# Kernel tuning notes

Hardware: AMD Instinct MI355X
Metric: run time of the kernel (lower is better)

## Reference

```python
import jax, jax.numpy as jnp
import numpy as np

B, S, D, H, HID = 2, 2048, 256, 8, 1024
EPS = 1e-9


def gelu_fast(x):
    return 0.5 * x * (1.0 + jnp.tanh(x * 0.7978845608 * (1.0 + 0.044715 * x * x)))


def layer_norm(x, g, b):
    m = jnp.mean(x, axis=-1, keepdims=True)
    v = jnp.mean(jnp.square(x - m), axis=-1, keepdims=True)
    return (x - m) * jax.lax.rsqrt(v + EPS) * g + b


def setup_inputs() -> dict:
    key = jax.random.key(0)
    ks = jax.random.split(key, 16)
    x = jax.random.normal(ks[0], (B, S, D), dtype=jnp.float32)
    # causal look-ahead mask: additive, 0 on/below diagonal, -1e9 above
    causal = jnp.triu(jnp.ones((S, S), dtype=jnp.float32), k=1) * (-1e9)
    look_ahead_mask = causal[None, None, :, :]  # (1,1,S,S)
    sd = 0.02
    return {
        "x": x,
        "look_ahead_mask": look_ahead_mask,
        "ln1_g": jnp.ones((D,), jnp.float32),
        "ln1_b": jnp.zeros((D,), jnp.float32),
        "wq_w": jax.random.normal(ks[1], (D * H, D), jnp.float32) * sd,
        "wq_b": jnp.zeros((D * H,), jnp.float32),
        "wk_w": jax.random.normal(ks[2], (D * H, D), jnp.float32) * sd,
        "wk_b": jnp.zeros((D * H,), jnp.float32),
        "wv_w": jax.random.normal(ks[3], (D * H, D), jnp.float32) * sd,
        "wv_b": jnp.zeros((D * H,), jnp.float32),
        "dense_w": jax.random.normal(ks[4], (D, D * H), jnp.float32) * sd,
        "dense_b": jnp.zeros((D,), jnp.float32),
        "ln2_g": jnp.ones((D,), jnp.float32),
        "ln2_b": jnp.zeros((D,), jnp.float32),
        "fc1_w": jax.random.normal(ks[5], (HID, D), jnp.float32) * sd,
        "fc1_b": jnp.zeros((HID,), jnp.float32),
        "fc2_w": jax.random.normal(ks[6], (D, HID), jnp.float32) * sd,
        "fc2_b": jnp.zeros((D,), jnp.float32),
    }


def reference(x, look_ahead_mask, ln1_g, ln1_b, wq_w, wq_b, wk_w, wk_b,
              wv_w, wv_b, dense_w, dense_b, ln2_g, ln2_b,
              fc1_w, fc1_b, fc2_w, fc2_b):
    xn = layer_norm(x, ln1_g, ln1_b)
    # QKV: D -> D*H, each head has full head-dim D (module quirk)
    q = (jnp.einsum('bsd,ed->bse', xn, wq_w) + wq_b).reshape(B, S, H, D).transpose(0, 2, 1, 3)
    k = (jnp.einsum('bsd,ed->bse', xn, wk_w) + wk_b).reshape(B, S, H, D).transpose(0, 2, 1, 3)
    v = (jnp.einsum('bsd,ed->bse', xn, wv_w) + wv_b).reshape(B, S, H, D).transpose(0, 2, 1, 3)
    scores = jnp.einsum('bhqd,bhkd->bhqk', q, k) / jnp.sqrt(jnp.float32(D))
    scores = scores + look_ahead_mask
    attn_weights = jax.nn.softmax(scores, axis=-1)
    ctx = jnp.einsum('bhqk,bhkd->bhqd', attn_weights, v)  # (B,H,S,D)
    ctx = ctx.transpose(0, 2, 1, 3).reshape(B, S, H * D)
    attn = jnp.einsum('bse,de->bsd', ctx, dense_w) + dense_b
    x1 = xn + attn  # residual uses post-LN x (module quirk)
    m = layer_norm(x1, ln2_g, ln2_b)
    m = gelu_fast(jnp.einsum('bsd,hd->bsh', m, fc1_w) + fc1_b)
    m = jnp.einsum('bsh,dh->bsd', m, fc2_w) + fc2_b
    out = x1 + m
    return out, attn_weights
```

## Files before the change

### kernel.cpp

```cpp
#include <hip/hip_runtime.h>
#include <hip/hip_bf16.h>


typedef __bf16 bf16_t;
typedef __bf16 bf16x8 __attribute__((ext_vector_type(8)));
typedef __bf16 bf16x4 __attribute__((ext_vector_type(4)));
typedef float  f32x4  __attribute__((ext_vector_type(4)));

#define DEV __device__ __forceinline__

DEV f32x4 mfma16(bf16x8 a, bf16x8 b, f32x4 c) {
  return __builtin_amdgcn_mfma_f32_16x16x32_bf16(a, b, c, 0, 0, 0);
}

DEV void gload16(const void* g, void* l) {
  __builtin_amdgcn_global_load_lds(
      (const __attribute__((address_space(1))) unsigned int*)g,
      (__attribute__((address_space(3))) unsigned int*)l, 16, 0, 0);
}

__global__ __launch_bounds__(256) void k1_lncvt(
    const float* __restrict__ x, const float* __restrict__ g, const float* __restrict__ bta,
    float* __restrict__ of, bf16_t* __restrict__ ob,
    const float* __restrict__ s0, const float* __restrict__ s1,
// ... 88 lines not shown
__global__ __launch_bounds__(256, 4) void gemm_qkv(
    const bf16_t* __restrict__ A,
    const bf16_t* __restrict__ W0, const bf16_t* __restrict__ W1, const bf16_t* __restrict__ W2,
    const float* __restrict__ b0, const float* __restrict__ b1, const float* __restrict__ b2,
    bf16_t* __restrict__ qo, bf16_t* __restrict__ ko, bf16_t* __restrict__ vto) {
  __shared__ char smem[34816];
  char* Asb = smem;
  char* Bsb = smem + 16384;
  int bx = blockIdx.x;
  int wsel = bx >> 4, cb = bx & 15;
  const bf16_t* W    = wsel == 0 ? W0 : (wsel == 1 ? W1 : W2);
  const float*  bias = wsel == 0 ? b0 : (wsel == 1 ? b1 : b2);
  int row0 = blockIdx.y * 128, col0 = cb * 128;
  f32x4 acc[4][4] = {};
  gemm_core(A, W, 256, row0, col0, 0, 8, Asb, Bsb, acc);

  int tid = threadIdx.x, w = tid >> 6, l = tid & 63, l15 = l & 15, lhi = l >> 4;
  int wr = (w >> 1) * 64, wc = (w & 1) * 64;

  if (wsel < 2) {
    bf16_t* out = wsel == 0 ? qo : ko;
#pragma unroll
    for (int m = 0; m < 4; ++m)
#pragma unroll
      for (int n = 0; n < 4; ++n)
#pragma unroll
        for (int j = 0; j < 4; ++j) {
          int row = row0 + wr + 16 * m + lhi * 4 + j;
          int col = col0 + wc + 16 * n + l15;
          float v = acc[m][n][j] + bias[col];
          out[((size_t)((row >> 11) * 8 + (col >> 8)) * 2048 + (row & 2047)) * 256 + (col & 255)] = (bf16_t)v;
        }
  } else {
    __syncthreads();
    bf16_t* T = (bf16_t*)smem;
#pragma unroll
    for (int m = 0; m < 4; ++m)
#pragma unroll
      for (int n = 0; n < 4; ++n) {
        int d = wc + 16 * n + l15;
        int s = wr + 16 * m + lhi * 4;
        bf16x4 v4;
#pragma unroll
        for (int j = 0; j < 4; ++j) v4[j] = (bf16_t)(acc[m][n][j] + bias[col0 + d]);
        *(bf16x4*)(T + d * 136 + s) = v4;
      }
    __syncthreads();
    int bh = ((row0 >> 11) << 3) + (col0 >> 8);
    int d0 = col0 & 255, s0g = row0 & 2047;
#pragma unroll
    for (int p = 0; p < 8; ++p) {
      int idx = p * 256 + tid;
      int d = idx >> 4, c = (idx & 15) * 8;
      bf16x8 v8 = *(const bf16x8*)(T + d * 136 + c);
      *(bf16x8*)(vto + ((size_t)bh * 256 + d0 + d) * 2048 + s0g + c) = v8;
    }
  }
}

__global__ __launch_bounds__(256, 4) void gemm_part(
    const bf16_t* __restrict__ A, const bf16_t* __restrict__ W,
    int lda, int ksub, float* __restrict__ parts) {
  __shared__ char Asb[2 * 8192];
  __shared__ char Bsb[2 * 8192];
  int z = blockIdx.z;
  int row0 = blockIdx.y * 128, col0 = blockIdx.x * 128;
  f32x4 acc[4][4] = {};
  gemm_core(A, W, lda, row0, col0, z * ksub, ksub >> 5, Asb, Bsb, acc);

  int tid = threadIdx.x, w = tid >> 6, l = tid & 63, l15 = l & 15, lhi = l >> 4;
  int wr = (w >> 1) * 64, wc = (w & 1) * 64;
  float* p = parts + (size_t)z * 1048576;
#pragma unroll
  for (int m = 0; m < 4; ++m)
#pragma unroll
    for (int n = 0; n < 4; ++n)
#pragma unroll
      for (int j = 0; j < 4; ++j) {
        int row = row0 + wr + 16 * m + lhi * 4 + j;
        int col = col0 + wc + 16 * n + l15;
        p[(size_t)row * 256 + col] = acc[m][n][j];
      }
}

__global__ __launch_bounds__(256) void reduce4(
    const float* __restrict__ parts, const float* __restrict__ bias,
    const float* __restrict__ res, float* __restrict__ out) {
  int i = blockIdx.x * 256 + threadIdx.x;
  f32x4 s = *(const f32x4*)(parts + (size_t)i * 4);
  s += *(const f32x4*)(parts + 1048576 + (size_t)i * 4);
  s += *(const f32x4*)(parts + 2097152 + (size_t)i * 4);
  s += *(const f32x4*)(parts + 3145728 + (size_t)i * 4);
  s += *(const f32x4*)(res + (size_t)i * 4);
  s += *(const f32x4*)(bias + (i & 63) * 4);
  *(f32x4*)(out + (size_t)i * 4) = s;
}

__global__ __launch_bounds__(256) void reduce_ln(
    const float* __restrict__ parts, const float* __restrict__ bias,
    const float* __restrict__ res, const float* __restrict__ g,
    const float* __restrict__ bta, float* __restrict__ x1o, bf16_t* __restrict__ mo) {
  int row = blockIdx.x * 4 + (threadIdx.x >> 6);
  int l = threadIdx.x & 63;
  size_t base = (size_t)row * 256 + l * 4;
  f32x4 s = *(const f32x4*)(parts + base);
  s += *(const f32x4*)(parts + 1048576 + base);
  s += *(const f32x4*)(parts + 2097152 + base);
  s += *(const f32x4*)(parts + 3145728 + base);
  s += *(const f32x4*)(res + base);
  s += *(const f32x4*)(bias + l * 4);
  *(f32x4*)(x1o + base) = s;
  float sm = s[0] + s[1] + s[2] + s[3];
  float s2 = s[0]*s[0] + s[1]*s[1] + s[2]*s[2] + s[3]*s[3];
#pragma unroll
  for (int o = 1; o < 64; o <<= 1) { sm += __shfl_xor(sm, o, 64); s2 += __shfl_xor(s2, o, 64); }
  float m   = sm * (1.f/256.f);
  float var = s2 * (1.f/256.f) - m * m;
  float rs  = rsqrtf(var + 1e-9f);
  const float4 gv = *(const float4*)(g   + l * 4);
  const float4 bv = *(const float4*)(bta + l * 4);
  bf16x4 yb;
  yb[0] = (bf16_t)((s[0] - m) * rs * gv.x + bv.x);
  yb[1] = (bf16_t)((s[1] - m) * rs * gv.y + bv.y);
  yb[2] = (bf16_t)((s[2] - m) * rs * gv.z + bv.z);
  yb[3] = (bf16_t)((s[3] - m) * rs * gv.w + bv.w);
  *(bf16x4*)(mo + base) = yb;
}

__global__ __launch_bounds__(256, 4) void gemm_fc1(
    const bf16_t* __restrict__ A, const bf16_t* __restrict__ W,
    const float* __restrict__ bias, bf16_t* __restrict__ out) {
  __shared__ char Asb[2 * 8192];
  __shared__ char Bsb[2 * 8192];
  int row0 = blockIdx.y * 128, col0 = blockIdx.x * 128;
  f32x4 acc[4][4] = {};
  gemm_core(A, W, 256, row0, col0, 0, 8, Asb, Bsb, acc);

  int tid = threadIdx.x, w = tid >> 6, l = tid & 63, l15 = l & 15, lhi = l >> 4;
  int wr = (w >> 1) * 64, wc = (w & 1) * 64;
#pragma unroll
  for (int m = 0; m < 4; ++m)
#pragma unroll
    for (int n = 0; n < 4; ++n)
#pragma unroll
      for (int j = 0; j < 4; ++j) {
        int row = row0 + wr + 16 * m + lhi * 4 + j;
        int col = col0 + wc + 16 * n + l15;
        float t = acc[m][n][j] + bias[col];
        float ge = 0.5f * t * (1.f + tanhf(0.7978845608f * t * (1.f + 0.044715f * t * t)));
        out[(size_t)row * 1024 + col] = (bf16_t)ge;
      }
}

__global__ __launch_bounds__(256, 2) void rowsum_k(
    const bf16_t* __restrict__ qg, const bf16_t* __restrict__ kg,
    float* __restrict__ rsg) {
  __shared__ bf16_t Ksh[2][64 * 256];
  __shared__ float  sl[2][64];
  int bx = blockIdx.x;
  int bh = bx & 15, qt = 31 - (bx >> 4);
  int tid = threadIdx.x, w = tid >> 6, l = tid & 63;
  int l15 = l & 15, lhi = l >> 4;
  int wm = w >> 1, wn = w & 1;
  const bf16_t* Q   = qg + (size_t)bh * 2048 * 256;
  const bf16_t* Kg2 = kg + (size_t)bh * 2048 * 256;
  int qbase = qt * 64;
  int nkt = qt + 1;

  bf16x8 qf[2][8];
#pragma unroll
  for (int m = 0; m < 2; ++m)
#pragma unroll
    for (int ks = 0; ks < 8; ++ks)
      qf[m][ks] = *(const bf16x8*)(Q + (size_t)(qbase + wm * 32 + m * 16 + l15) * 256 + ks * 32 + lhi * 8);

#define RSTAGE(t_) do {                                                        \
    char* dst = (char*)Ksh[(t_) & 1] + w * 1024;                               \
    _Pragma("unroll")                                                          \
    for (int j = 0; j < 8; ++j) {                                              \
      int idx = (j * 256 + tid) * 16; int r = idx >> 9;                        \
      int co = (idx & 511) ^ ((r & 7) << 4);                                   \
      gload16(Kg2 + (size_t)((t_) * 64 + r) * 256 + (co >> 1), dst + j * 4096);\
    } } while (0)

  RSTAGE(0);
  if (nkt > 1) RSTAGE(1);

  float sums[2][4] = {};
  for (int t = 0; t < nkt; ++t) {
    if (t + 1 < nkt) asm volatile("s_waitcnt vmcnt(8)" ::: "memory");
    else             asm volatile("s_waitcnt vmcnt(0)" ::: "memory");
    __builtin_amdgcn_s_barrier();
    const char* Kb = (const char*)Ksh[t & 1];
    f32x4 acc[2][2] = {};
    __builtin_amdgcn_s_setprio(1);
#pragma unroll
    for (int ks = 0; ks < 8; ++ks) {
#pragma unroll
      for (int n2 = 0; n2 < 2; ++n2) {
        int row = wn * 32 + n2 * 16 + l15;
        bf16x8 kb = *(const bf16x8*)(Kb + row * 512 + ((ks * 64 + lhi * 16) ^ ((row & 7) << 4)));
#pragma unroll
        for (int m = 0; m < 2; ++m)
          acc[m][n2] = mfma16(qf[m][ks], kb, acc[m][n2]);
      }
    }
    __builtin_amdgcn_s_setprio(0);
#pragma unroll
    for (int m = 0; m < 2; ++m)
#pragma unroll
      for (int n2 = 0; n2 < 2; ++n2)
#pragma unroll
        for (int j = 0; j < 4; ++j) {
          int qr = qbase + wm * 32 + m * 16 + lhi * 4 + j;
          int kc = t * 64 + wn * 32 + n2 * 16 + l15;
          sums[m][j] += (kc <= qr) ? __expf(acc[m][n2][j] * 0.0625f) : 0.f;
        }
    asm volatile("s_waitcnt lgkmcnt(0)" ::: "memory");
    __builtin_amdgcn_s_barrier();
    if (t + 2 < nkt) RSTAGE(t + 2);
  }
#undef RSTAGE

#pragma unroll
  for (int m = 0; m < 2; ++m)
#pragma unroll
    for (int j = 0; j < 4; ++j) {
#pragma unroll
      for (int o = 1; o < 16; o <<= 1) sums[m][j] += __shfl_xor(sums[m][j], o, 64);
    }
  if (l15 == 0) {
#pragma unroll
    for (int m = 0; m < 2; ++m)
#pragma unroll
      for (int j = 0; j < 4; ++j)
        sl[wn][wm * 32 + m * 16 + lhi * 4 + j] = sums[m][j];
  }
  __syncthreads();
  if (tid < 64)
    rsg[(size_t)bh * 2048 + qbase + tid] = 1.f / (sl[0][tid] + sl[1][tid]);
}

__global__ __launch_bounds__(256, 2) void attn_pv(
    const bf16_t* __restrict__ qg, const bf16_t* __restrict__ kg,
    const bf16_t* __restrict__ vt, const float* __restrict__ rsg,
    float* __restrict__ pout, bf16_t* __restrict__ ctxo) {
  __shared__ bf16_t Ksh[2][32 * 256];
  __shared__ bf16_t Vsh[2][256 * 32];
  __shared__ bf16_t Psh[64 * 32];
  int bx = blockIdx.x;
  int bh = bx & 15, qt = 31 - (bx >> 4);
  int tid = threadIdx.x, w = tid >> 6, l = tid & 63;
  int l15 = l & 15, lhi = l >> 4;
  int wm = w >> 1, wn = w & 1;
  const bf16_t* Q   = qg + (size_t)bh * 2048 * 256;
  const bf16_t* Kg2 = kg + (size_t)bh * 2048 * 256;
  const bf16_t* Vt  = vt + (size_t)bh * 256 * 2048;
  int qbase = qt * 64;
  int nkt = 2 * (qt + 1);

  bf16x8 qf[2][8];
#pragma unroll
  for (int m = 0; m < 2; ++m)
#pragma unroll
    for (int ks = 0; ks < 8; ++ks)
      qf[m][ks] = *(const bf16x8*)(Q + (size_t)(qbase + wm * 32 + m * 16 + l15) * 256 + ks * 32 + lhi * 8);

  float inv[8];
#pragma unroll
  for (int m = 0; m < 2; ++m)
#pragma unroll
    for (int j = 0; j < 4; ++j)
      inv[m * 4 + j] = rsg[(size_t)bh * 2048 + qbase + wm * 32 + m * 16 + lhi * 4 + j];

#define PSTAGE(t_) do {                                                         \
    char* kd = (char*)Ksh[(t_) & 1] + w * 1024;                                 \
    char* vd = (char*)Vsh[(t_) & 1] + w * 1024;                                 \
    _Pragma("unroll")                                                           \
    for (int j = 0; j < 4; ++j) {                                               \
      int idx = (j * 256 + tid) * 16;                                           \
      { int r = idx >> 9; int co = (idx & 511) ^ ((r & 7) << 4);                \
        gload16(Kg2 + (size_t)((t_) * 32 + r) * 256 + (co >> 1), kd + j * 4096); } \
      { int r = idx >> 6; int co = (idx & 63) ^ (((r >> 2) & 3) << 4);          \
        gload16(Vt + (size_t)r * 2048 + (t_) * 32 + (co >> 1), vd + j * 4096); } \
    } } while (0)

  PSTAGE(0);
  PSTAGE(1);

  f32x4 ctx[4][4] = {};
  for (int t = 0; t < nkt; ++t) {
    if (t + 1 < nkt) asm volatile("s_waitcnt vmcnt(8)" ::: "memory");
    else             asm volatile("s_waitcnt vmcnt(0)" ::: "memory");
    __builtin_amdgcn_s_barrier();
    const char* Kb = (const char*)Ksh[t & 1];
    const char* Vb = (const char*)Vsh[t & 1];

    f32x4 acc[2] = {};
    __builtin_amdgcn_s_setprio(1);
#pragma unroll
    for (int ks = 0; ks < 8; ++ks) {
      int row = wn * 16 + l15;
      bf16x8 kb = *(const bf16x8*)(Kb + row * 512 + ((ks * 64 + lhi * 16) ^ ((row & 7) << 4)));
#pragma unroll
      for (int m = 0; m < 2; ++m)
        acc[m] = mfma16(qf[m][ks], kb, acc[m]);
    }
    __builtin_amdgcn_s_setprio(0);
#pragma unroll
    for (int m = 0; m < 2; ++m)
#pragma unroll
      for (int j = 0; j < 4; ++j) {
        int rr = wm * 32 + m * 16 + lhi * 4 + j;
        int qr = qbase + rr;
        int kc = t * 32 + wn * 16 + l15;
        float e = (kc <= qr) ? __expf(acc[m][j] * 0.0625f) * inv[m * 4 + j] : 0.f;
        int addr = rr * 64 + (wn * 16 + l15) * 2;
        *(bf16_t*)((char*)Psh + (addr ^ (((rr >> 2) & 3) << 4))) = (bf16_t)e;
      }
    asm volatile("s_waitcnt lgkmcnt(0)" ::: "memory");
    __builtin_amdgcn_s_barrier();

    {
      int row = tid >> 2;
      int ch  = (tid & 3) * 16;
      bf16x8 p8 = *(const bf16x8*)((const char*)Psh + row * 64 + (ch ^ (((row >> 2) & 3) << 4)));
      float* dst = pout + ((size_t)bh * 2048 + qbase + row) * 2048 + t * 32 + (tid & 3) * 8;
      f32x4 lo = { (float)p8[0], (float)p8[1], (float)p8[2], (float)p8[3] };
      f32x4 hi = { (float)p8[4], (float)p8[5], (float)p8[6], (float)p8[7] };
      *(f32x4*)dst = lo;
      *(f32x4*)(dst + 4) = hi;
    }

    bf16x8 pa[4], vb[4];
#pragma unroll
    for (int m4 = 0; m4 < 4; ++m4) {
      int row = m4 * 16 + l15;
      pa[m4] = *(const bf16x8*)((const char*)Psh + ((row * 64 + lhi * 16) ^ (((row >> 2) & 3) << 4)));
    }
#pragma unroll
    for (int n = 0; n < 4; ++n) {
      int row = w * 64 + n * 16 + l15;
      vb[n] = *(const bf16x8*)(Vb + ((row * 64 + lhi * 16) ^ (((row >> 2) & 3) << 4)));
    }
    __builtin_amdgcn_s_setprio(1);
#pragma unroll
    for (int m4 = 0; m4 < 4; ++m4)
#pragma unroll
      for (int n = 0; n < 4; ++n)
        ctx[m4][n] = mfma16(pa[m4], vb[n], ctx[m4][n]);
    __builtin_amdgcn_s_setprio(0);

    asm volatile("s_waitcnt lgkmcnt(0)" ::: "memory");
    __builtin_amdgcn_s_barrier();
    if (t + 2 < nkt) PSTAGE(t + 2);
  }
#undef PSTAGE

  int b = bh >> 3, h = bh & 7;
#pragma unroll
  for (int m4 = 0; m4 < 4; ++m4)
#pragma unroll
    for (int n = 0; n < 4; ++n)
#pragma unroll
      for (int j = 0; j < 4; ++j) {
        int qr = qbase + m4 * 16 + lhi * 4 + j;
        ctxo[((size_t)b * 2048 + qr) * 2048 + h * 256 + w * 64 + n * 16 + l15] = (bf16_t)ctx[m4][n][j];
      }

  int zs = qbase + 64;
  for (int r = 0; r < 64; ++r) {
    size_t base = ((size_t)bh * 2048 + qbase + r) * 2048;
    for (int c = zs + tid * 4; c < 2048; c += 1024) {
      *(float4*)(pout + base + c) = make_float4(0.f, 0.f, 0.f, 0.f);
    }
  }
}

extern "C" void kernel_launch(void* const* d_in, const int* in_sizes, int n_in,
                              void* d_out, int out_size, void* d_ws, size_t ws_size,
                              hipStream_t stream) {
  const float* x     = (const float*)d_in[0];
  const float* ln1g  = (const float*)d_in[2];
  const float* ln1b  = (const float*)d_in[3];
  const float* wq_w  = (const float*)d_in[4];
  const float* wq_b  = (const float*)d_in[5];
  const float* wk_w  = (const float*)d_in[6];
  const float* wk_b  = (const float*)d_in[7];
  const float* wv_w  = (const float*)d_in[8];
  const float* wv_b  = (const float*)d_in[9];
  const float* dw    = (const float*)d_in[10];
  const float* db    = (const float*)d_in[11];
  const float* ln2g  = (const float*)d_in[12];
  const float* ln2b  = (const float*)d_in[13];
  const float* f1w   = (const float*)d_in[14];
  const float* f1b   = (const float*)d_in[15];
  const float* f2w   = (const float*)d_in[16];
  const float* f2b   = (const float*)d_in[17];

  char* ws = (char*)d_ws;
  const size_t MB = 1u << 20;
  float*  xn_f = (float*) (ws + 0 * MB);
  bf16_t* xn_b = (bf16_t*)(ws + 4 * MB);
  bf16_t* q_b  = (bf16_t*)(ws + 6 * MB);
  bf16_t* k_b  = (bf16_t*)(ws + 22 * MB);
  bf16_t* ctx_b= (bf16_t*)(ws + 38 * MB);
  bf16_t* vt_b = (bf16_t*)(ws + 54 * MB);
  float*  x1_f = (float*) (ws + 70 * MB);
  bf16_t* m_b  = (bf16_t*)(ws + 74 * MB);
  bf16_t* h_b  = (bf16_t*)(ws + 76 * MB);
  bf16_t* wq_bf = (bf16_t*)(ws + 84 * MB);
  bf16_t* wk_bf = wq_bf + 524288;
  bf16_t* wv_bf = wk_bf + 524288;
  bf16_t* dw_bf = wv_bf + 524288;
  bf16_t* f1_bf = dw_bf + 524288;
  bf16_t* f2_bf = f1_bf + 262144;
  float*  rs_f  = (float*)(ws + 90 * MB);
  float* parts_d = (float*)q_b;
  float* parts_f = (float*)k_b;

  float* out0 = (float*)d_out;
  float* pout = out0 + 1048576;

  k1_lncvt<<<3584, 256, 0, stream>>>(x, ln1g, ln1b, xn_f, xn_b,
                                     wq_w, wk_w, wv_w, dw, f1w, f2w,
                                     wq_bf, wk_bf, wv_bf, dw_bf, f1_bf, f2_bf);

  gemm_qkv<<<dim3(48, 32), 256, 0, stream>>>(xn_b, wq_bf, wk_bf, wv_bf,
                                             wq_b, wk_b, wv_b, q_b, k_b, vt_b);

  rowsum_k<<<512, 256, 0, stream>>>(q_b, k_b, rs_f);

  attn_pv<<<512, 256, 0, stream>>>(q_b, k_b, vt_b, rs_f, pout, ctx_b);

  gemm_part<<<dim3(2, 32, 4), 256, 0, stream>>>(ctx_b, dw_bf, 2048, 512, parts_d);
  reduce_ln<<<1024, 256, 0, stream>>>(parts_d, db, xn_f, ln2g, ln2b, x1_f, m_b);

  gemm_fc1<<<dim3(8, 32), 256, 0, stream>>>(m_b, f1_bf, f1b, h_b);

  gemm_part<<<dim3(2, 32, 4), 256, 0, stream>>>(h_b, f2_bf, 1024, 256, parts_f);
  reduce4<<<1024, 256, 0, stream>>>(parts_f, f2b, x1_f, out0);
}
```

Measured before the change: 217.5 us.

## Fuse softmax rowsum pass into PV attention kernel with 32-row query tiles

Merges the separate row-sum kernel and the probability/PV kernel into one kernel that first computes the causal exp row sums for its query tile, then reuses the same shared memory to produce probabilities, write the attention weights and accumulate context. Query tiles shrink from 64 to 32 rows and the grid doubles to 1024 blocks, which improves load balance on the causal triangle and removes one launch and the global rowsum round trip. In exchange each block recomputes QK^T twice over fewer rows, and K/V tiles are reused across fewer query rows, so K and V global traffic roughly doubles.

```diff
diff --git a/kernel.cpp b/kernel.cpp
--- a/kernel.cpp
+++ b/kernel.cpp
@@ -264,130 +264,102 @@
       }
 }
 
-__global__ __launch_bounds__(256, 2) void rowsum_k(
+__global__ __launch_bounds__(256, 2) void attn_fused(
     const bf16_t* __restrict__ qg, const bf16_t* __restrict__ kg,
-    float* __restrict__ rsg) {
-  __shared__ bf16_t Ksh[2][64 * 256];
-  __shared__ float  sl[2][64];
+    const bf16_t* __restrict__ vt, float* __restrict__ pout,
+    bf16_t* __restrict__ ctxo) {
+  __shared__ __align__(16) char smem[67712];
   int bx = blockIdx.x;
-  int bh = bx & 15, qt = 31 - (bx >> 4);
+  int bh = bx & 15, qt = 63 - (bx >> 4);
   int tid = threadIdx.x, w = tid >> 6, l = tid & 63;
   int l15 = l & 15, lhi = l >> 4;
-  int wm = w >> 1, wn = w & 1;
   const bf16_t* Q   = qg + (size_t)bh * 2048 * 256;
   const bf16_t* Kg2 = kg + (size_t)bh * 2048 * 256;
-  int qbase = qt * 64;
-  int nkt = qt + 1;
+  const bf16_t* Vt  = vt + (size_t)bh * 256 * 2048;
+  int qbase = qt * 32;
+  float* sl    = (float*)(smem + 65536);
+  float* invsh = (float*)(smem + 67584);
 
   bf16x8 qf[2][8];
 #pragma unroll
   for (int m = 0; m < 2; ++m)
 #pragma unroll
     for (int ks = 0; ks < 8; ++ks)
-      qf[m][ks] = *(const bf16x8*)(Q + (size_t)(qbase + wm * 32 + m * 16 + l15) * 256 + ks * 32 + lhi * 8);
-
-#define RSTAGE(t_) do {                                                        \
-    char* dst = (char*)Ksh[(t_) & 1] + w * 1024;                               \
+      qf[m][ks] = *(const bf16x8*)(Q + (size_t)(qbase + m * 16 + l15) * 256 + ks * 32 + lhi * 8);
+
+  char* KA = smem;
+  int nktA = (qt >> 1) + 1;
+#define ASTAGE(t_) do {                                                        \
+    char* dst = KA + ((t_) & 1) * 32768 + w * 1024;                            \
     _Pragma("unroll")                                                          \
     for (int j = 0; j < 8; ++j) {                                              \
       int idx = (j * 256 + tid) * 16; int r = idx >> 9;                        \
       int co = (idx & 511) ^ ((r & 7) << 4);                                   \
       gload16(Kg2 + (size_t)((t_) * 64 + r) * 256 + (co >> 1), dst + j * 4096);\
     } } while (0)
-
-  RSTAGE(0);
-  if (nkt > 1) RSTAGE(1);
+  ASTAGE(0);
+  if (nktA > 1) ASTAGE(1);
 
   float sums[2][4] = {};
-  for (int t = 0; t < nkt; ++t) {
-    if (t + 1 < nkt) asm volatile("s_waitcnt vmcnt(8)" ::: "memory");
-    else             asm volatile("s_waitcnt vmcnt(0)" ::: "memory");
-    __builtin_amdgcn_s_barrier();
-    const char* Kb = (const char*)Ksh[t & 1];
-    f32x4 acc[2][2] = {};
+  for (int t = 0; t < nktA; ++t) {
+    if (t + 1 < nktA) asm volatile("s_waitcnt vmcnt(8)" ::: "memory");
+    else              asm volatile("s_waitcnt vmcnt(0)" ::: "memory");
+    __builtin_amdgcn_s_barrier();
+    const char* Kb = KA + (t & 1) * 32768;
+    int row = w * 16 + l15;
+    f32x4 acc[2] = {};
     __builtin_amdgcn_s_setprio(1);
 #pragma unroll
     for (int ks = 0; ks < 8; ++ks) {
-#pragma unroll
-      for (int n2 = 0; n2 < 2; ++n2) {
-        int row = wn * 32 + n2 * 16 + l15;
-        bf16x8 kb = *(const bf16x8*)(Kb + row * 512 + ((ks * 64 + lhi * 16) ^ ((row & 7) << 4)));
-#pragma unroll
-        for (int m = 0; m < 2; ++m)
-          acc[m][n2] = mfma16(qf[m][ks], kb, acc[m][n2]);
+      bf16x8 kb = *(const bf16x8*)(Kb + row * 512 + ((ks * 64 + lhi * 16) ^ ((row & 7) << 4)));
+      acc[0] = mfma16(qf[0][ks], kb, acc[0]);
+      acc[1] = mfma16(qf[1][ks], kb, acc[1]);
+    }
+    __builtin_amdgcn_s_setprio(0);
+#pragma unroll
+    for (int m = 0; m < 2; ++m)
+#pragma unroll
+      for (int j = 0; j < 4; ++j) {
+        int qr = qbase + m * 16 + lhi * 4 + j;
+        int kc = t * 64 + row;
+        sums[m][j] += (kc <= qr) ? __expf(acc[m][j] * 0.0625f) : 0.f;
       }
-    }
-    __builtin_amdgcn_s_setprio(0);
+    asm volatile("s_waitcnt lgkmcnt(0)" ::: "memory");
+    __builtin_amdgcn_s_barrier();
+    if (t + 2 < nktA) ASTAGE(t + 2);
+  }
+#undef ASTAGE
+
+#pragma unroll
+  for (int m = 0; m < 2; ++m)
+#pragma unroll
+    for (int j = 0; j < 4; ++j)
+#pragma unroll
+      for (int o = 1; o < 16; o <<= 1)
+        sums[m][j] += __shfl_xor(sums[m][j], o, 64);
+  if (l15 == 0)
 #pragma unroll
     for (int m = 0; m < 2; ++m)
 #pragma unroll
-      for (int n2 = 0; n2 < 2; ++n2)
-#pragma unroll
-        for (int j = 0; j < 4; ++j) {
-          int qr = qbase + wm * 32 + m * 16 + lhi * 4 + j;
-          int kc = t * 64 + wn * 32 + n2 * 16 + l15;
-          sums[m][j] += (kc <= qr) ? __expf(acc[m][n2][j] * 0.0625f) : 0.f;
-        }
-    asm volatile("s_waitcnt lgkmcnt(0)" ::: "memory");
-    __builtin_amdgcn_s_barrier();
-    if (t + 2 < nkt) RSTAGE(t + 2);
-  }
-#undef RSTAGE
-
-#pragma unroll
-  for (int m = 0; m < 2; ++m)
-#pragma unroll
-    for (int j = 0; j < 4; ++j) {
-#pragma unroll
-      for (int o = 1; o < 16; o <<= 1) sums[m][j] += __shfl_xor(sums[m][j], o, 64);
-    }
-  if (l15 == 0) {
-#pragma unroll
-    for (int m = 0; m < 2; ++m)
-#pragma unroll
       for (int j = 0; j < 4; ++j)
-        sl[wn][wm * 32 + m * 16 + lhi * 4 + j] = sums[m][j];
-  }
+        sl[w * 32 + m * 16 + lhi * 4 + j] = sums[m][j];
   __syncthreads();
-  if (tid < 64)
-    rsg[(size_t)bh * 2048 + qbase + tid] = 1.f / (sl[0][tid] + sl[1][tid]);
-}
-
-__global__ __launch_bounds__(256, 2) void attn_pv(
-    const bf16_t* __restrict__ qg, const bf16_t* __restrict__ kg,
-    const bf16_t* __restrict__ vt, const float* __restrict__ rsg,
-    float* __restrict__ pout, bf16_t* __restrict__ ctxo) {
-  __shared__ bf16_t Ksh[2][32 * 256];
-  __shared__ bf16_t Vsh[2][256 * 32];
-  __shared__ bf16_t Psh[64 * 32];
-  int bx = blockIdx.x;
-  int bh = bx & 15, qt = 31 - (bx >> 4);
-  int tid = threadIdx.x, w = tid >> 6, l = tid & 63;
-  int l15 = l & 15, lhi = l >> 4;
+  if (tid < 32)
+    invsh[tid] = 1.f / (sl[tid] + sl[32 + tid] + sl[64 + tid] + sl[96 + tid]);
+  __syncthreads();
+
+  char* KB  = smem;
+  char* VB  = smem + 32768;
+  char* Psh = smem + 65536;
   int wm = w >> 1, wn = w & 1;
-  const bf16_t* Q   = qg + (size_t)bh * 2048 * 256;
-  const bf16_t* Kg2 = kg + (size_t)bh * 2048 * 256;
-  const bf16_t* Vt  = vt + (size_t)bh * 256 * 2048;
-  int qbase = qt * 64;
-  int nkt = 2 * (qt + 1);
-
-  bf16x8 qf[2][8];
-#pragma unroll
-  for (int m = 0; m < 2; ++m)
-#pragma unroll
-    for (int ks = 0; ks < 8; ++ks)
-      qf[m][ks] = *(const bf16x8*)(Q + (size_t)(qbase + wm * 32 + m * 16 + l15) * 256 + ks * 32 + lhi * 8);
-
-  float inv[8];
-#pragma unroll
-  for (int m = 0; m < 2; ++m)
-#pragma unroll
-    for (int j = 0; j < 4; ++j)
-      inv[m * 4 + j] = rsg[(size_t)bh * 2048 + qbase + wm * 32 + m * 16 + lhi * 4 + j];
-
-#define PSTAGE(t_) do {                                                         \
-    char* kd = (char*)Ksh[(t_) & 1] + w * 1024;                                 \
-    char* vd = (char*)Vsh[(t_) & 1] + w * 1024;                                 \
+  float inv4[4];
+#pragma unroll
+  for (int j = 0; j < 4; ++j) inv4[j] = invsh[wm * 16 + lhi * 4 + j];
+
+  int nktB = qt + 1;
+#define BSTAGE(t_) do {                                                         \
+    char* kd = KB + ((t_) & 1) * 16384 + w * 1024;                              \
+    char* vd = VB + ((t_) & 1) * 16384 + w * 1024;                              \
     _Pragma("unroll")                                                           \
     for (int j = 0; j < 4; ++j) {                                               \
       int idx = (j * 256 + tid) * 16;                                           \
@@ -396,96 +368,87 @@
       { int r = idx >> 6; int co = (idx & 63) ^ (((r >> 2) & 3) << 4);          \
         gload16(Vt + (size_t)r * 2048 + (t_) * 32 + (co >> 1), vd + j * 4096); } \
     } } while (0)
-
-  PSTAGE(0);
-  PSTAGE(1);
-
-  f32x4 ctx[4][4] = {};
-  for (int t = 0; t < nkt; ++t) {
-    if (t + 1 < nkt) asm volatile("s_waitcnt vmcnt(8)" ::: "memory");
-    else             asm volatile("s_waitcnt vmcnt(0)" ::: "memory");
-    __builtin_amdgcn_s_barrier();
-    const char* Kb = (const char*)Ksh[t & 1];
-    const char* Vb = (const char*)Vsh[t & 1];
-
-    f32x4 acc[2] = {};
+  BSTAGE(0);
+  if (nktB > 1) BSTAGE(1);
+
+  f32x4 ctx[2][4] = {};
+  for (int t = 0; t < nktB; ++t) {
+    if (t + 1 >= nktB)      asm volatile("s_waitcnt vmcnt(0)" ::: "memory");
+    else if (t == 0)        asm volatile("s_waitcnt vmcnt(8)" ::: "memory");
+    else                    asm volatile("s_waitcnt vmcnt(9)" ::: "memory");
+    __builtin_amdgcn_s_barrier();
+    const char* Kb = KB + (t & 1) * 16384;
+    const char* Vb = VB + (t & 1) * 16384;
+
+    f32x4 acc = {};
+    int krow = wn * 16 + l15;
     __builtin_amdgcn_s_setprio(1);
 #pragma unroll
     for (int ks = 0; ks < 8; ++ks) {
-      int row = wn * 16 + l15;
-      bf16x8 kb = *(const bf16x8*)(Kb + row * 512 + ((ks * 64 + lhi * 16) ^ ((row & 7) << 4)));
-#pragma unroll
-      for (int m = 0; m < 2; ++m)
-        acc[m] = mfma16(qf[m][ks], kb, acc[m]);
+      bf16x8 kb = *(const bf16x8*)(Kb + krow * 512 + ((ks * 64 + lhi * 16) ^ ((krow & 7) << 4)));
+      acc = mfma16(qf[wm][ks], kb, acc);
     }
     __builtin_amdgcn_s_setprio(0);
 #pragma unroll
+    for (int j = 0; j < 4; ++j) {
+      int rr = wm * 16 + lhi * 4 + j;
+      int qr = qbase + rr;
+      int kc = t * 32 + krow;
+      float e = (kc <= qr) ? __expf(acc[j] * 0.0625f) * inv4[j] : 0.f;
+      int addr = rr * 64 + krow * 2;
+      *(bf16_t*)(Psh + (addr ^ (((rr >> 2) & 3) << 4))) = (bf16_t)e;
+    }
+    asm volatile("s_waitcnt lgkmcnt(0)" ::: "memory");
+    __builtin_amdgcn_s_barrier();
+
+    bf16x8 pa[2], vb[4];
+#pragma unroll
+    for (int m = 0; m < 2; ++m) {
+      int pr = m * 16 + l15;
+      pa[m] = *(const bf16x8*)(Psh + ((pr * 64 + lhi * 16) ^ (((pr >> 2) & 3) << 4)));
+    }
+#pragma unroll
+    for (int n = 0; n < 4; ++n) {
+      int vr = w * 64 + n * 16 + l15;
+      vb[n] = *(const bf16x8*)(Vb + ((vr * 64 + lhi * 16) ^ (((vr >> 2) & 3) << 4)));
+    }
+    __builtin_amdgcn_s_setprio(1);
+#pragma unroll
     for (int m = 0; m < 2; ++m)
 #pragma unroll
+      for (int n = 0; n < 4; ++n)
+        ctx[m][n] = mfma16(pa[m], vb[n], ctx[m][n]);
+    __builtin_amdgcn_s_setprio(0);
+
+    {
+      int prow = tid >> 3, chunk = tid & 7;
+      const char* src = Psh + prow * 64 + ((chunk * 8) ^ (((prow >> 2) & 3) << 4));
+      bf16x4 p4 = *(const bf16x4*)src;
+      f32x4 o = { (float)p4[0], (float)p4[1], (float)p4[2], (float)p4[3] };
+      *(f32x4*)(pout + ((size_t)bh * 2048 + qbase + prow) * 2048 + t * 32 + chunk * 4) = o;
+    }
+    asm volatile("s_waitcnt lgkmcnt(0)" ::: "memory");
+    __builtin_amdgcn_s_barrier();
+    if (t + 2 < nktB) BSTAGE(t + 2);
+  }
+#undef BSTAGE
+
+  int b = bh >> 3, h = bh & 7;
+#pragma unroll
+  for (int m = 0; m < 2; ++m)
+#pragma unroll
+    for (int n = 0; n < 4; ++n)
+#pragma unroll
       for (int j = 0; j < 4; ++j) {
-        int rr = wm * 32 + m * 16 + lhi * 4 + j;
-        int qr = qbase + rr;
-        int kc = t * 32 + wn * 16 + l15;
-        float e = (kc <= qr) ? __expf(acc[m][j] * 0.0625f) * inv[m * 4 + j] : 0.f;
-        int addr = rr * 64 + (wn * 16 + l15) * 2;
-        *(bf16_t*)((char*)Psh + (addr ^ (((rr >> 2) & 3) << 4))) = (bf16_t)e;
+        int qr = qbase + m * 16 + lhi * 4 + j;
+        ctxo[((size_t)b * 2048 + qr) * 2048 + h * 256 + w * 64 + n * 16 + l15] = (bf16_t)ctx[m][n][j];
       }
-    asm volatile("s_waitcnt lgkmcnt(0)" ::: "memory");
-    __builtin_amdgcn_s_barrier();
-
-    {
-      int row = tid >> 2;
-      int ch  = (tid & 3) * 16;
-      bf16x8 p8 = *(const bf16x8*)((const char*)Psh + row * 64 + (ch ^ (((row >> 2) & 3) << 4)));
-      float* dst = pout + ((size_t)bh * 2048 + qbase + row) * 2048 + t * 32 + (tid & 3) * 8;
-      f32x4 lo = { (float)p8[0], (float)p8[1], (float)p8[2], (float)p8[3] };
-      f32x4 hi = { (float)p8[4], (float)p8[5], (float)p8[6], (float)p8[7] };
-      *(f32x4*)dst = lo;
-      *(f32x4*)(dst + 4) = hi;
-    }
-
-    bf16x8 pa[4], vb[4];
-#pragma unroll
-    for (int m4 = 0; m4 < 4; ++m4) {
-      int row = m4 * 16 + l15;
-      pa[m4] = *(const bf16x8*)((const char*)Psh + ((row * 64 + lhi * 16) ^ (((row >> 2) & 3) << 4)));
-    }
-#pragma unroll
-    for (int n = 0; n < 4; ++n) {
-      int row = w * 64 + n * 16 + l15;
-      vb[n] = *(const bf16x8*)(Vb + ((row * 64 + lhi * 16) ^ (((row >> 2) & 3) << 4)));
-    }
-    __builtin_amdgcn_s_setprio(1);
-#pragma unroll
-    for (int m4 = 0; m4 < 4; ++m4)
-#pragma unroll
-      for (int n = 0; n < 4; ++n)
-        ctx[m4][n] = mfma16(pa[m4], vb[n], ctx[m4][n]);
-    __builtin_amdgcn_s_setprio(0);
-
-    asm volatile("s_waitcnt lgkmcnt(0)" ::: "memory");
-    __builtin_amdgcn_s_barrier();
-    if (t + 2 < nkt) PSTAGE(t + 2);
-  }
-#undef PSTAGE
-
-  int b = bh >> 3, h = bh & 7;
-#pragma unroll
-  for (int m4 = 0; m4 < 4; ++m4)
-#pragma unroll
-    for (int n = 0; n < 4; ++n)
-#pragma unroll
-      for (int j = 0; j < 4; ++j) {
-        int qr = qbase + m4 * 16 + lhi * 4 + j;
-        ctxo[((size_t)b * 2048 + qr) * 2048 + h * 256 + w * 64 + n * 16 + l15] = (bf16_t)ctx[m4][n][j];
-      }
-
-  int zs = qbase + 64;
-  for (int r = 0; r < 64; ++r) {
-    size_t base = ((size_t)bh * 2048 + qbase + r) * 2048;
-    for (int c = zs + tid * 4; c < 2048; c += 1024) {
-      *(float4*)(pout + base + c) = make_float4(0.f, 0.f, 0.f, 0.f);
-    }
+
+  int zs = qbase + 32;
+  for (int r = 0; r < 32; ++r) {
+    size_t base2 = ((size_t)bh * 2048 + qbase + r) * 2048;
+    for (int c = zs + tid * 4; c < 2048; c += 1024)
+      *(float4*)(pout + base2 + c) = make_float4(0.f, 0.f, 0.f, 0.f);
   }
 }
 
@@ -527,7 +490,6 @@
   bf16_t* dw_bf = wv_bf + 524288;
   bf16_t* f1_bf = dw_bf + 524288;
   bf16_t* f2_bf = f1_bf + 262144;
-  float*  rs_f  = (float*)(ws + 90 * MB);
   float* parts_d = (float*)q_b;
   float* parts_f = (float*)k_b;
 
@@ -541,9 +503,7 @@
   gemm_qkv<<<dim3(48, 32), 256, 0, stream>>>(xn_b, wq_bf, wk_bf, wv_bf,
                                              wq_b, wk_b, wv_b, q_b, k_b, vt_b);
 
-  rowsum_k<<<512, 256, 0, stream>>>(q_b, k_b, rs_f);
-
-  attn_pv<<<512, 256, 0, stream>>>(q_b, k_b, vt_b, rs_f, pout, ctx_b);
+  attn_fused<<<1024, 256, 0, stream>>>(q_b, k_b, vt_b, pout, ctx_b);
 
   gemm_part<<<dim3(2, 32, 4), 256, 0, stream>>>(ctx_b, dw_bf, 2048, 512, parts_d);
   reduce_ln<<<1024, 256, 0, stream>>>(parts_d, db, xn_f, ln2g, ln2b, x1_f, m_b);
```

Measured after the change: 236.6 us. 1.09x slower.

## Restructure causal attention PV kernel around 64-key tiles with register-loaded V

Applied to the files above, without the earlier changes.

The attention kernel now processes 64-key tiles instead of 32. Only K is staged into double-buffered LDS, with a 16-row XOR swizzle. V fragments are loaded straight from global memory into registers, and P is double-buffered, so each iteration needs one fewer barrier. Query-tile ordering is also remapped so that the first half of the grid runs the longest tiles in descending order and the second half runs the short ones in ascending order. The aim is to halve loop-iteration and synchronisation overhead and improve load balance, at the cost of more LDS per block (80 KB) and more register pressure from the V fragments and accumulators.

```diff
diff --git a/kernel.cpp b/kernel.cpp
--- a/kernel.cpp
+++ b/kernel.cpp
@@ -357,19 +357,21 @@
     const bf16_t* __restrict__ qg, const bf16_t* __restrict__ kg,
     const bf16_t* __restrict__ vt, const float* __restrict__ rsg,
     float* __restrict__ pout, bf16_t* __restrict__ ctxo) {
-  __shared__ bf16_t Ksh[2][32 * 256];
-  __shared__ bf16_t Vsh[2][256 * 32];
-  __shared__ bf16_t Psh[64 * 32];
+  __shared__ __align__(16) char smem[81920];
+  char* Ksh = smem;
+  char* Psh = smem + 65536;
   int bx = blockIdx.x;
-  int bh = bx & 15, qt = 31 - (bx >> 4);
+  int bh = bx & 15;
+  int qt = (bx < 256) ? (31 - (bx >> 4)) : ((bx - 256) >> 4);
+  int qbase = qt * 64;
+  int nkt = qt + 1;
+
   int tid = threadIdx.x, w = tid >> 6, l = tid & 63;
   int l15 = l & 15, lhi = l >> 4;
   int wm = w >> 1, wn = w & 1;
-  const bf16_t* Q   = qg + (size_t)bh * 2048 * 256;
-  const bf16_t* Kg2 = kg + (size_t)bh * 2048 * 256;
-  const bf16_t* Vt  = vt + (size_t)bh * 256 * 2048;
-  int qbase = qt * 64;
-  int nkt = 2 * (qt + 1);
+  const bf16_t* Q = qg + (size_t)bh * 2048 * 256;
+  const bf16_t* K = kg + (size_t)bh * 2048 * 256;
+  const bf16_t* V = vt + (size_t)bh * 256 * 2048;
 
   bf16x8 qf[2][8];
 #pragma unroll
@@ -378,114 +380,120 @@
     for (int ks = 0; ks < 8; ++ks)
       qf[m][ks] = *(const bf16x8*)(Q + (size_t)(qbase + wm * 32 + m * 16 + l15) * 256 + ks * 32 + lhi * 8);
 
-  float inv[8];
+  float inv4[2][4];
 #pragma unroll
   for (int m = 0; m < 2; ++m)
 #pragma unroll
     for (int j = 0; j < 4; ++j)
-      inv[m * 4 + j] = rsg[(size_t)bh * 2048 + qbase + wm * 32 + m * 16 + lhi * 4 + j];
-
-#define PSTAGE(t_) do {                                                         \
-    char* kd = (char*)Ksh[(t_) & 1] + w * 1024;                                 \
-    char* vd = (char*)Vsh[(t_) & 1] + w * 1024;                                 \
-    _Pragma("unroll")                                                           \
-    for (int j = 0; j < 4; ++j) {                                               \
-      int idx = (j * 256 + tid) * 16;                                           \
-      { int r = idx >> 9; int co = (idx & 511) ^ ((r & 7) << 4);                \
-        gload16(Kg2 + (size_t)((t_) * 32 + r) * 256 + (co >> 1), kd + j * 4096); } \
-      { int r = idx >> 6; int co = (idx & 63) ^ (((r >> 2) & 3) << 4);          \
-        gload16(Vt + (size_t)r * 2048 + (t_) * 32 + (co >> 1), vd + j * 4096); } \
+      inv4[m][j] = rsg[(size_t)bh * 2048 + qbase + wm * 32 + m * 16 + lhi * 4 + j];
+
+#define KSTAGE(td_, ts_) do {                                                  \
+    char* dst0 = Ksh + ((td_) & 1) * 32768 + w * 8192;                         \
+    _Pragma("unroll")                                                          \
+    for (int j5 = 0; j5 < 8; ++j5) {                                           \
+      int idxb = w * 8192 + j5 * 1024 + (tid & 63) * 16;                       \
+      int r5 = idxb >> 9; int inner = idxb & 511;                              \
+      int colb = inner ^ ((r5 & 15) << 4);                                     \
+      gload16(K + (size_t)((ts_) * 64 + r5) * 256 + (colb >> 1), dst0 + j5 * 1024); \
     } } while (0)
 
-  PSTAGE(0);
-  PSTAGE(1);
+  KSTAGE(0, 0);
+  asm volatile("s_waitcnt vmcnt(0)" ::: "memory");
+  __builtin_amdgcn_s_barrier();
 
   f32x4 ctx[4][4] = {};
   for (int t = 0; t < nkt; ++t) {
-    if (t + 1 < nkt) asm volatile("s_waitcnt vmcnt(8)" ::: "memory");
-    else             asm volatile("s_waitcnt vmcnt(0)" ::: "memory");
+    int tn = (t + 1 < nkt) ? t + 1 : nkt - 1;
+    KSTAGE(t + 1, tn);
+    bf16x8 vb[4][2];
+#pragma unroll
+    for (int n4 = 0; n4 < 4; ++n4)
+#pragma unroll
+      for (int ks2 = 0; ks2 < 2; ++ks2)
+        vb[n4][ks2] = *(const bf16x8*)(V + (size_t)(w * 64 + n4 * 16 + l15) * 2048 + t * 64 + ks2 * 32 + lhi * 8);
+
+    const char* Kb = Ksh + (t & 1) * 32768;
+    f32x4 acc[2][2] = {};
+    __builtin_amdgcn_s_setprio(1);
+#pragma unroll
+    for (int ks = 0; ks < 8; ++ks) {
+#pragma unroll
+      for (int n2 = 0; n2 < 2; ++n2) {
+        int krow = wn * 32 + n2 * 16 + l15;
+        bf16x8 kb = *(const bf16x8*)(Kb + krow * 512 + ((ks * 64 + lhi * 16) ^ ((krow & 15) << 4)));
+#pragma unroll
+        for (int m = 0; m < 2; ++m)
+          acc[m][n2] = mfma16(qf[m][ks], kb, acc[m][n2]);
+      }
+    }
+    __builtin_amdgcn_s_setprio(0);
+
+    char* Pb = Psh + (t & 1) * 8192;
+#pragma unroll
+    for (int m = 0; m < 2; ++m)
+#pragma unroll
+      for (int n2 = 0; n2 < 2; ++n2)
+#pragma unroll
+        for (int j = 0; j < 4; ++j) {
+          int rr = wm * 32 + m * 16 + lhi * 4 + j;
+          int cc = wn * 32 + n2 * 16 + l15;
+          int qr = qbase + rr;
+          int kc = t * 64 + cc;
+          float e = (kc <= qr) ? __expf(acc[m][n2][j] * 0.0625f) * inv4[m][j] : 0.f;
+          *(bf16_t*)(Pb + rr * 128 + ((cc * 2) ^ ((rr & 7) << 4))) = (bf16_t)e;
+        }
+    asm volatile("s_waitcnt lgkmcnt(0)" ::: "memory");
+    asm volatile("s_waitcnt vmcnt(8)" ::: "memory");
     __builtin_amdgcn_s_barrier();
-    const char* Kb = (const char*)Ksh[t & 1];
-    const char* Vb = (const char*)Vsh[t & 1];
-
-    f32x4 acc[2] = {};
+
+    {
+      int prow = tid >> 2, c0 = (tid & 3) * 16;
+      float* dst = pout + ((size_t)bh * 2048 + qbase + prow) * 2048 + t * 64 + c0;
+#pragma unroll
+      for (int h8 = 0; h8 < 2; ++h8) {
+        bf16x8 p8 = *(const bf16x8*)(Pb + prow * 128 + (((c0 + h8 * 8) * 2) ^ ((prow & 7) << 4)));
+        f32x4 lo = { (float)p8[0], (float)p8[1], (float)p8[2], (float)p8[3] };
+        f32x4 hi = { (float)p8[4], (float)p8[5], (float)p8[6], (float)p8[7] };
+        *(f32x4*)(dst + h8 * 8) = lo;
+        *(f32x4*)(dst + h8 * 8 + 4) = hi;
+      }
+    }
+
     __builtin_amdgcn_s_setprio(1);
 #pragma unroll
-    for (int ks = 0; ks < 8; ++ks) {
-      int row = wn * 16 + l15;
-      bf16x8 kb = *(const bf16x8*)(Kb + row * 512 + ((ks * 64 + lhi * 16) ^ ((row & 7) << 4)));
-#pragma unroll
-      for (int m = 0; m < 2; ++m)
-        acc[m] = mfma16(qf[m][ks], kb, acc[m]);
+    for (int ks2 = 0; ks2 < 2; ++ks2) {
+      bf16x8 pa[4];
+#pragma unroll
+      for (int m4 = 0; m4 < 4; ++m4) {
+        int pr = m4 * 16 + l15;
+        pa[m4] = *(const bf16x8*)(Pb + pr * 128 + (((ks2 * 64 + lhi * 16)) ^ ((pr & 7) << 4)));
+      }
+#pragma unroll
+      for (int m4 = 0; m4 < 4; ++m4)
+#pragma unroll
+        for (int n4 = 0; n4 < 4; ++n4)
+          ctx[m4][n4] = mfma16(pa[m4], vb[n4][ks2], ctx[m4][n4]);
     }
     __builtin_amdgcn_s_setprio(0);
-#pragma unroll
-    for (int m = 0; m < 2; ++m)
-#pragma unroll
-      for (int j = 0; j < 4; ++j) {
-        int rr = wm * 32 + m * 16 + lhi * 4 + j;
-        int qr = qbase + rr;
-        int kc = t * 32 + wn * 16 + l15;
-        float e = (kc <= qr) ? __expf(acc[m][j] * 0.0625f) * inv[m * 4 + j] : 0.f;
-        int addr = rr * 64 + (wn * 16 + l15) * 2;
-        *(bf16_t*)((char*)Psh + (addr ^ (((rr >> 2) & 3) << 4))) = (bf16_t)e;
-      }
-    asm volatile("s_waitcnt lgkmcnt(0)" ::: "memory");
-    __builtin_amdgcn_s_barrier();
-
-    {
-      int row = tid >> 2;
-      int ch  = (tid & 3) * 16;
-      bf16x8 p8 = *(const bf16x8*)((const char*)Psh + row * 64 + (ch ^ (((row >> 2) & 3) << 4)));
-      float* dst = pout + ((size_t)bh * 2048 + qbase + row) * 2048 + t * 32 + (tid & 3) * 8;
-      f32x4 lo = { (float)p8[0], (float)p8[1], (float)p8[2], (float)p8[3] };
-      f32x4 hi = { (float)p8[4], (float)p8[5], (float)p8[6], (float)p8[7] };
-      *(f32x4*)dst = lo;
-      *(f32x4*)(dst + 4) = hi;
-    }
-
-    bf16x8 pa[4], vb[4];
-#pragma unroll
-    for (int m4 = 0; m4 < 4; ++m4) {
-      int row = m4 * 16 + l15;
-      pa[m4] = *(const bf16x8*)((const char*)Psh + ((row * 64 + lhi * 16) ^ (((row >> 2) & 3) << 4)));
-    }
-#pragma unroll
-    for (int n = 0; n < 4; ++n) {
-      int row = w * 64 + n * 16 + l15;
-      vb[n] = *(const bf16x8*)(Vb + ((row * 64 + lhi * 16) ^ (((row >> 2) & 3) << 4)));
-    }
-    __builtin_amdgcn_s_setprio(1);
-#pragma unroll
-    for (int m4 = 0; m4 < 4; ++m4)
-#pragma unroll
-      for (int n = 0; n < 4; ++n)
-        ctx[m4][n] = mfma16(pa[m4], vb[n], ctx[m4][n]);
-    __builtin_amdgcn_s_setprio(0);
-
-    asm volatile("s_waitcnt lgkmcnt(0)" ::: "memory");
-    __builtin_amdgcn_s_barrier();
-    if (t + 2 < nkt) PSTAGE(t + 2);
-  }
-#undef PSTAGE
+  }
+#undef KSTAGE
 
   int b = bh >> 3, h = bh & 7;
 #pragma unroll
   for (int m4 = 0; m4 < 4; ++m4)
 #pragma unroll
-    for (int n = 0; n < 4; ++n)
+    for (int n4 = 0; n4 < 4; ++n4)
 #pragma unroll
       for (int j = 0; j < 4; ++j) {
         int qr = qbase + m4 * 16 + lhi * 4 + j;
-        ctxo[((size_t)b * 2048 + qr) * 2048 + h * 256 + w * 64 + n * 16 + l15] = (bf16_t)ctx[m4][n][j];
+        ctxo[((size_t)b * 2048 + qr) * 2048 + h * 256 + w * 64 + n4 * 16 + l15] = (bf16_t)ctx[m4][n4][j];
       }
 
   int zs = qbase + 64;
   for (int r = 0; r < 64; ++r) {
-    size_t base = ((size_t)bh * 2048 + qbase + r) * 2048;
-    for (int c = zs + tid * 4; c < 2048; c += 1024) {
-      *(float4*)(pout + base + c) = make_float4(0.f, 0.f, 0.f, 0.f);
-    }
+    size_t base2 = ((size_t)bh * 2048 + qbase + r) * 2048;
+    for (int c = zs + tid * 4; c < 2048; c += 1024)
+      *(float4*)(pout + base2 + c) = make_float4(0.f, 0.f, 0.f, 0.f);
   }
 }
 
```

Result: slower. 266.6 us (+22.6%).

## Restructure attention PV loop with double-buffered P and direct register stores

Applied to the files above, without the earlier changes.

The attn_pv kernel now double-buffers the P tile in shared memory. It drops the barrier at the top of the loop and issues the next K/V prefetch right after the softmax barrier, so prefetch depth goes from two stages ahead to one. Attention probabilities are written to global memory straight from registers in fp32 instead of being re-read from LDS as bf16 and stored as vectors. The aim is to remove one LDS round-trip and one barrier per iteration. In exchange it uses narrower, less coalesced global stores and a shallower prefetch pipeline.

```diff
diff --git a/kernel.cpp b/kernel.cpp
--- a/kernel.cpp
+++ b/kernel.cpp
@@ -357,19 +357,21 @@
     const bf16_t* __restrict__ qg, const bf16_t* __restrict__ kg,
     const bf16_t* __restrict__ vt, const float* __restrict__ rsg,
     float* __restrict__ pout, bf16_t* __restrict__ ctxo) {
-  __shared__ bf16_t Ksh[2][32 * 256];
-  __shared__ bf16_t Vsh[2][256 * 32];
-  __shared__ bf16_t Psh[64 * 32];
+  __shared__ __align__(16) bf16_t Ksh[2][32 * 256];
+  __shared__ __align__(16) bf16_t Vsh[2][256 * 32];
+  __shared__ __align__(16) bf16_t Psh[2][64 * 32];
   int bx = blockIdx.x;
-  int bh = bx & 15, qt = 31 - (bx >> 4);
+  int bh = bx & 15;
+  int qt = (bx < 256) ? (31 - (bx >> 4)) : ((bx - 256) >> 4);
+  int qbase = qt * 64;
+  int nkt = 2 * (qt + 1);
+
   int tid = threadIdx.x, w = tid >> 6, l = tid & 63;
   int l15 = l & 15, lhi = l >> 4;
   int wm = w >> 1, wn = w & 1;
-  const bf16_t* Q   = qg + (size_t)bh * 2048 * 256;
-  const bf16_t* Kg2 = kg + (size_t)bh * 2048 * 256;
-  const bf16_t* Vt  = vt + (size_t)bh * 256 * 2048;
-  int qbase = qt * 64;
-  int nkt = 2 * (qt + 1);
+  const bf16_t* Q  = qg + (size_t)bh * 2048 * 256;
+  const bf16_t* K  = kg + (size_t)bh * 2048 * 256;
+  const bf16_t* Vt = vt + (size_t)bh * 256 * 2048;
 
   bf16x8 qf[2][8];
 #pragma unroll
@@ -378,12 +380,12 @@
     for (int ks = 0; ks < 8; ++ks)
       qf[m][ks] = *(const bf16x8*)(Q + (size_t)(qbase + wm * 32 + m * 16 + l15) * 256 + ks * 32 + lhi * 8);
 
-  float inv[8];
+  float inv4[2][4];
 #pragma unroll
   for (int m = 0; m < 2; ++m)
 #pragma unroll
     for (int j = 0; j < 4; ++j)
-      inv[m * 4 + j] = rsg[(size_t)bh * 2048 + qbase + wm * 32 + m * 16 + lhi * 4 + j];
+      inv4[m][j] = rsg[(size_t)bh * 2048 + qbase + wm * 32 + m * 16 + lhi * 4 + j];
 
 #define PSTAGE(t_) do {                                                         \
     char* kd = (char*)Ksh[(t_) & 1] + w * 1024;                                 \
@@ -392,68 +394,68 @@
     for (int j = 0; j < 4; ++j) {                                               \
       int idx = (j * 256 + tid) * 16;                                           \
       { int r = idx >> 9; int co = (idx & 511) ^ ((r & 7) << 4);                \
-        gload16(Kg2 + (size_t)((t_) * 32 + r) * 256 + (co >> 1), kd + j * 4096); } \
+        gload16(K + (size_t)((t_) * 32 + r) * 256 + (co >> 1), kd + j * 4096); }\
       { int r = idx >> 6; int co = (idx & 63) ^ (((r >> 2) & 3) << 4);          \
-        gload16(Vt + (size_t)r * 2048 + (t_) * 32 + (co >> 1), vd + j * 4096); } \
+        gload16(Vt + (size_t)r * 2048 + (t_) * 32 + (co >> 1), vd + j * 4096); }\
     } } while (0)
 
   PSTAGE(0);
-  PSTAGE(1);
-
+  asm volatile("s_waitcnt vmcnt(0)" ::: "memory");
+  __builtin_amdgcn_s_barrier();
+
+  int krow = wn * 16 + l15;
   f32x4 ctx[4][4] = {};
   for (int t = 0; t < nkt; ++t) {
-    if (t + 1 < nkt) asm volatile("s_waitcnt vmcnt(8)" ::: "memory");
-    else             asm volatile("s_waitcnt vmcnt(0)" ::: "memory");
-    __builtin_amdgcn_s_barrier();
     const char* Kb = (const char*)Ksh[t & 1];
     const char* Vb = (const char*)Vsh[t & 1];
+    char* Pb = (char*)Psh[t & 1];
 
     f32x4 acc[2] = {};
     __builtin_amdgcn_s_setprio(1);
 #pragma unroll
     for (int ks = 0; ks < 8; ++ks) {
-      int row = wn * 16 + l15;
-      bf16x8 kb = *(const bf16x8*)(Kb + row * 512 + ((ks * 64 + lhi * 16) ^ ((row & 7) << 4)));
-#pragma unroll
-      for (int m = 0; m < 2; ++m)
-        acc[m] = mfma16(qf[m][ks], kb, acc[m]);
+      bf16x8 kb = *(const bf16x8*)(Kb + krow * 512 + ((ks * 64 + lhi * 16) ^ ((krow & 7) << 4)));
+      acc[0] = mfma16(qf[0][ks], kb, acc[0]);
+      acc[1] = mfma16(qf[1][ks], kb, acc[1]);
     }
     __builtin_amdgcn_s_setprio(0);
+
+    float ev[2][4];
 #pragma unroll
     for (int m = 0; m < 2; ++m)
 #pragma unroll
       for (int j = 0; j < 4; ++j) {
         int rr = wm * 32 + m * 16 + lhi * 4 + j;
         int qr = qbase + rr;
-        int kc = t * 32 + wn * 16 + l15;
-        float e = (kc <= qr) ? __expf(acc[m][j] * 0.0625f) * inv[m * 4 + j] : 0.f;
-        int addr = rr * 64 + (wn * 16 + l15) * 2;
-        *(bf16_t*)((char*)Psh + (addr ^ (((rr >> 2) & 3) << 4))) = (bf16_t)e;
+        int kc = t * 32 + krow;
+        float e = (kc <= qr) ? __expf(acc[m][j] * 0.0625f) * inv4[m][j] : 0.f;
+        ev[m][j] = e;
+        int addr = rr * 64 + krow * 2;
+        *(bf16_t*)((char*)Pb + (addr ^ (((rr >> 2) & 3) << 4))) = (bf16_t)e;
       }
     asm volatile("s_waitcnt lgkmcnt(0)" ::: "memory");
     __builtin_amdgcn_s_barrier();
 
-    {
-      int row = tid >> 2;
-      int ch  = (tid & 3) * 16;
-      bf16x8 p8 = *(const bf16x8*)((const char*)Psh + row * 64 + (ch ^ (((row >> 2) & 3) << 4)));
-      float* dst = pout + ((size_t)bh * 2048 + qbase + row) * 2048 + t * 32 + (tid & 3) * 8;
-      f32x4 lo = { (float)p8[0], (float)p8[1], (float)p8[2], (float)p8[3] };
-      f32x4 hi = { (float)p8[4], (float)p8[5], (float)p8[6], (float)p8[7] };
-      *(f32x4*)dst = lo;
-      *(f32x4*)(dst + 4) = hi;
-    }
+    if (t + 1 < nkt) PSTAGE(t + 1);
+
+#pragma unroll
+    for (int m = 0; m < 2; ++m)
+#pragma unroll
+      for (int j = 0; j < 4; ++j) {
+        int rr = wm * 32 + m * 16 + lhi * 4 + j;
+        pout[((size_t)bh * 2048 + qbase + rr) * 2048 + t * 32 + krow] = ev[m][j];
+      }
 
     bf16x8 pa[4], vb[4];
 #pragma unroll
     for (int m4 = 0; m4 < 4; ++m4) {
-      int row = m4 * 16 + l15;
-      pa[m4] = *(const bf16x8*)((const char*)Psh + ((row * 64 + lhi * 16) ^ (((row >> 2) & 3) << 4)));
+      int pr = m4 * 16 + l15;
+      pa[m4] = *(const bf16x8*)((const char*)Pb + ((pr * 64 + lhi * 16) ^ (((pr >> 2) & 3) << 4)));
     }
 #pragma unroll
     for (int n = 0; n < 4; ++n) {
-      int row = w * 64 + n * 16 + l15;
-      vb[n] = *(const bf16x8*)(Vb + ((row * 64 + lhi * 16) ^ (((row >> 2) & 3) << 4)));
+      int vr = w * 64 + n * 16 + l15;
+      vb[n] = *(const bf16x8*)((const char*)Vb + ((vr * 64 + lhi * 16) ^ (((vr >> 2) & 3) << 4)));
     }
     __builtin_amdgcn_s_setprio(1);
 #pragma unroll
@@ -464,8 +466,8 @@
     __builtin_amdgcn_s_setprio(0);
 
     asm volatile("s_waitcnt lgkmcnt(0)" ::: "memory");
+    asm volatile("s_waitcnt vmcnt(8)" ::: "memory");
     __builtin_amdgcn_s_barrier();
-    if (t + 2 < nkt) PSTAGE(t + 2);
   }
 #undef PSTAGE
 
@@ -482,10 +484,9 @@
 
   int zs = qbase + 64;
   for (int r = 0; r < 64; ++r) {
-    size_t base = ((size_t)bh * 2048 + qbase + r) * 2048;
-    for (int c = zs + tid * 4; c < 2048; c += 1024) {
-      *(float4*)(pout + base + c) = make_float4(0.f, 0.f, 0.f, 0.f);
-    }
+    size_t base2 = ((size_t)bh * 2048 + qbase + r) * 2048;
+    for (int c = zs + tid * 4; c < 2048; c += 1024)
+      *(float4*)(pout + base2 + c) = make_float4(0.f, 0.f, 0.f, 0.f);
   }
 }
 
```

Result: slower. 225.2 us (+3.6%).
